# Optimization experiments

Measured on AMD Instinct MI355X. Metric: run time of the kernel, lower is better.

## Reference

```python
import jax, jax.numpy as jnp
import numpy as np

B, T, F, D, K, C, O = 256, 16, 8, 32, 64, 1024, 2

def setup_inputs():
    ks = jax.random.split(jax.random.key(0), 16)
    return {
        "tdata": jax.random.normal(ks[0], (B, T, F, D), jnp.float32),
        "f_mask": jax.random.randint(ks[1], (B, T, F), 0, 2, jnp.int32),
        "centers": jax.random.normal(ks[2], (F, K, D), jnp.float32),
        "pat": jax.random.randint(ks[3], (F, C, F), 0, K + 2, jnp.int32),
        "pat_rep": jax.random.normal(ks[4], (F, C, D), jnp.float32),
        "pos_cnt": jax.random.uniform(ks[5], (F, C), jnp.float32),
        "neg_cnt": jax.random.uniform(ks[6], (F, C), jnp.float32),
        "W_q": jax.random.normal(ks[7], (F, D, D), jnp.float32) * 0.1,
        "b_q": jax.random.normal(ks[8], (F, D), jnp.float32) * 0.1,
        "W_k": jax.random.normal(ks[9], (F, D, D + 1), jnp.float32) * 0.1,
        "b_k": jax.random.normal(ks[10], (F, D), jnp.float32) * 0.1,
        "W_v": jax.random.normal(ks[11], (F, D + 1, D + 1), jnp.float32) * 0.1,
        "b_v": jax.random.normal(ks[12], (F, D + 1), jnp.float32) * 0.1,
        "W_pred": jax.random.normal(ks[13], (O, F * (D + 1)), jnp.float32) * 0.1,
    }

def reference(tdata, f_mask, centers, pat, pat_rep, pos_cnt, neg_cnt,
              W_q, b_q, W_k, b_k, W_v, b_v, W_pred):
    Bv, Tv, Fv, Dv = tdata.shape
    BT = Bv * Tv
    fdata = tdata.reshape(BT, Fv, Dv)                     # [BT, F, D]

    # --- VQ nearest-centroid codes per feature (compute_codes) ---
    def codes_one(x, cen):                                # x [BT, D], cen [K, D]
        d = (jnp.sum(x * x, 1, keepdims=True)
             - 2.0 * (x @ cen.T)
             + jnp.sum(cen * cen, 1)[None, :])
        return jnp.argmin(d, axis=1)
    codes = jax.vmap(codes_one, in_axes=(1, 0), out_axes=1)(fdata, centers)  # [BT, F]
    mflat = f_mask.reshape(BT, Fv)
    # scatter_add equivalent: masked positions get code+2, unmasked get 1
    f_codes = jnp.where(mflat != 0, codes.astype(jnp.int32) + 2, 1)          # [BT, F]

    ratio = pos_cnt / (pos_cnt + neg_cnt + 1e-6)          # [F, C]
    rep = jnp.concatenate([pat_rep, ratio[..., None]], axis=-1)  # [F, C, D+1]
    query = tdata[:, -1]                                  # [B, F, D]

    def per_feature(pat_i, rep_i, q_i, Wq, bq, Wk, bk, Wv, bv):
        # pattern match: wildcard (0) always matches, else code must equal
        wild = pat_i == 0                                 # [C, F]
        eq = jnp.where(wild[None], True, f_codes[:, None, :] == pat_i[None])  # [BT, C, F]
        match = jnp.any(jnp.all(eq, axis=2).reshape(Bv, Tv, -1), axis=1)      # [B, C]
        key_t = match[..., None].astype(rep_i.dtype) * rep_i[None]            # [B, C, D+1]
        iq = q_i @ Wq.T + bq                              # [B, D]
        ik = key_t @ Wk.T + bk                            # [B, C, D]
        iv = key_t @ Wv.T + bv                            # [B, C, D+1]
        e = jnp.einsum('bcd,bd->bc', ik, iq)
        e = e - (1.0 - match.astype(e.dtype)) * 1e7
        a = jax.nn.softmax(e, axis=-1)
        v = jnp.einsum('bc,bcd->bd', a, iv)               # [B, D+1]
        return v, a

    v_all, a_all = jax.vmap(per_feature, in_axes=(0, 0, 1, 0, 0, 0, 0, 0, 0))(
        pat, rep, query, W_q, b_q, W_k, b_k, W_v, b_v)    # [F,B,D+1], [F,B,C]
    srep = jnp.swapaxes(v_all, 0, 1)                      # [B, F, D+1]
    fm = jnp.any(f_mask != 0, axis=1).astype(srep.dtype)  # [B, F]
    srep = srep * fm[..., None]
    cali = srep.reshape(Bv, -1) @ W_pred.T                # [B, O]
    return cali, a_all, srep
```

## Files before the change

### kernel.cpp

```cpp
#include <hip/hip_runtime.h>
#include <math.h>

#define Bv 256
#define Tv 16
#define Fv 8
#define Dv 32
#define Kv 64
#define Cv 1024
#define Ov 2
#define D1 33

typedef unsigned long long u64;
typedef unsigned char u8;

struct SM {
  float xsh[Tv * Fv * Dv];
  u64   cds[Tv];
  int   fmask[Tv * Fv];
  float srep_all[Fv * D1];
  float vsum[Fv][D1];
};

__global__ __launch_bounds__(512) void fused(
    const float* __restrict__ tdata, const int* __restrict__ f_mask,
    const float* __restrict__ centers, const int* __restrict__ pat,
    const float* __restrict__ pat_rep, const float* __restrict__ pos_cnt,
    const float* __restrict__ neg_cnt,
    const float* __restrict__ W_q, const float* __restrict__ b_q,
    const float* __restrict__ W_k, const float* __restrict__ b_k,
    const float* __restrict__ W_v, const float* __restrict__ b_v,
    const float* __restrict__ W_pred,
    float* __restrict__ cali, float* __restrict__ a_out,
    float* __restrict__ srep_out) {
  __shared__ SM sm;
  int b = blockIdx.x, tid = threadIdx.x;
  int w = tid >> 6, lane = tid & 63;

  {
    const float4* src = (const float4*)(tdata + (size_t)b * (Tv * Fv * Dv));
    float4* dst = (float4*)sm.xsh;
    dst[tid] = src[tid];
    dst[tid + 512] = src[tid + 512];
    if (tid < Tv * Fv) sm.fmask[tid] = f_mask[b * (Tv * Fv) + tid];
  }
  __syncthreads();

  {
    const float4* cp = (const float4*)(centers + (size_t)(w * Kv + lane) * Dv);
    float4 c4[8];
    float cc = 0.f;
    #pragma unroll
    for (int i = 0; i < 8; i++) {
      float4 v = cp[i];
      c4[i] = v;
      cc += v.x * v.x + v.y * v.y + v.z * v.z + v.w * v.w;
    }
    #pragma unroll
    for (int t = 0; t < Tv; t += 2) {
      const float4* x0 = (const float4*)&sm.xsh[(t * Fv + w) * Dv];
      const float4* x1 = (const float4*)&sm.xsh[((t + 1) * Fv + w) * Dv];
      float dot0 = 0.f, dot1 = 0.f;
      #pragma unroll
      for (int i = 0; i < 8; i++) {
        float4 a = x0[i], bq = x1[i];
        dot0 += c4[i].x * a.x + c4[i].y * a.y + c4[i].z * a.z + c4[i].w * a.w;
        dot1 += c4[i].x * bq.x + c4[i].y * bq.y + c4[i].z * bq.z + c4[i].w * bq.w;
      }
      float d0 = cc - 2.0f * dot0;
      float d1 = cc - 2.0f * dot1;
      float m0 = d0, m1 = d1;
      #pragma unroll
      for (int off = 1; off <= 32; off <<= 1) {
        m0 = fminf(m0, __shfl_xor(m0, off, 64));
        m1 = fminf(m1, __shfl_xor(m1, off, 64));
      }
      u64 bl0 = __ballot(d0 == m0);
      u64 bl1 = __ballot(d1 == m1);
      int k0 = __ffsll(bl0) - 1;
      int k1 = __ffsll(bl1) - 1;
      if (lane == 0) {
        ((u8*)sm.cds)[t * Fv + w] = sm.fmask[t * Fv + w] ? (u8)(k0 + 2) : (u8)1;
        ((u8*)sm.cds)[(t + 1) * Fv + w] = sm.fmask[(t + 1) * Fv + w] ? (u8)(k1 + 2) : (u8)1;
      }
    }
  }
  __syncthreads();

  int f = w;
  u64 creg[Tv];
  #pragma unroll
  for (int t = 0; t < Tv; t++) creg[t] = sm.cds[t];

  int fmlv = (lane < Tv) ? sm.fmask[lane * Fv + f] : 0;
  bool fm = __any(fmlv != 0);

  unsigned mask16 = 0u;
  #pragma unroll 4
  for (int jj = 0; jj < 16; jj++) {
    int c = (jj << 6) + lane;
    const int4* pr = (const int4*)(pat + ((size_t)f * Cv + c) * Fv);
    int4 pa = pr[0], pb = pr[1];
    int vals[8] = {pa.x, pa.y, pa.z, pa.w, pb.x, pb.y, pb.z, pb.w};
    u64 P = 0, M = 0;
    #pragma unroll
    for (int k = 0; k < 8; k++) {
      P |= ((u64)(vals[k] & 0xFF)) << (8 * k);
      if (vals[k] != 0) M |= 0xFFull << (8 * k);
    }
    u64 pm = P & M;
    bool m = false;
    #pragma unroll
    for (int t = 0; t < Tv; t++) m = m || ((creg[t] & M) == pm);
    if (m) mask16 |= (1u << jj);
  }
  bool anym = __any(mask16 != 0u);

  float* arow = a_out + (size_t)(f * Bv + b) * Cv;

  if (!anym) {
    const float uu = 1.0f / 1024.0f;
    #pragma unroll
    for (int jj = 0; jj < 16; jj++) arow[(jj << 6) + lane] = uu;
    if (lane < D1) {
      float vd = fm ? b_v[f * D1 + lane] : 0.f;
      srep_out[(b * Fv + f) * D1 + lane] = vd;
      sm.srep_all[f * D1 + lane] = vd;
    }
  } else {
    if (lane < D1) sm.vsum[f][lane] = 0.f;
    float iqv = 0.f;
    if (lane < Dv) {
      const float* wq = W_q + (f * Dv + lane) * Dv;
      const float* xq = &sm.xsh[((Tv - 1) * Fv + f) * Dv];
      float s = b_q[f * Dv + lane];
      for (int j = 0; j < Dv; j++) s += wq[j] * xq[j];
      iqv = s;
    }
    float zv = 0.f;
    for (int i = 0; i < Dv; i++) {
      float iqi = __shfl(iqv, i, 64);
      float coef = 0.f;
      if (lane < D1) coef = W_k[(f * Dv + i) * D1 + lane];
      else if (lane == D1) coef = b_k[f * Dv + i];
      zv += coef * iqi;
    }
    float ev[16];
    float lmax = -INFINITY;
    for (int jj = 0; jj < 16; jj++) {
      ev[jj] = 0.f;
      if (mask16 & (1u << jj)) {
        int c = (jj << 6) + lane;
        const float* rp = pat_rep + ((size_t)f * Cv + c) * Dv;
        float p = pos_cnt[f * Cv + c], n = neg_cnt[f * Cv + c];
        float r = p / (p + n + 1e-6f);
        float s = __shfl(zv, D1, 64) + r * __shfl(zv, Dv, 64);
        for (int j = 0; j < Dv; j++) s += rp[j] * __shfl(zv, j, 64);
        ev[jj] = s;
        lmax = fmaxf(lmax, s);
      }
    }
    float bm = lmax;
    #pragma unroll
    for (int off = 1; off <= 32; off <<= 1) bm = fmaxf(bm, __shfl_xor(bm, off, 64));
    float ls = 0.f;
    for (int jj = 0; jj < 16; jj++) {
      if (mask16 & (1u << jj)) { ev[jj] = expf(ev[jj] - bm); ls += ev[jj]; }
    }
    float Zs = ls;
    #pragma unroll
    for (int off = 1; off <= 32; off <<= 1) Zs += __shfl_xor(Zs, off, 64);
    for (int jj = 0; jj < 16; jj++) {
      int c = (jj << 6) + lane;
      bool hit = (mask16 & (1u << jj)) != 0u;
      float a = hit ? ev[jj] / Zs : 0.f;
      arow[c] = a;
      if (hit && a != 0.f) {
        const float* rp = pat_rep + ((size_t)f * Cv + c) * Dv;
        float p = pos_cnt[f * Cv + c], n = neg_cnt[f * Cv + c];
        float r = p / (p + n + 1e-6f);
        for (int j = 0; j < Dv; j++) atomicAdd(&sm.vsum[f][j], a * rp[j]);
        atomicAdd(&sm.vsum[f][Dv], a * r);
      }
    }
    if (lane < D1) {
      float s = b_v[f * D1 + lane];
      const float* wvp = W_v + (f * D1 + lane) * D1;
      for (int j = 0; j < D1; j++) s += wvp[j] * sm.vsum[f][j];
      float vd = fm ? s : 0.f;
      srep_out[(b * Fv + f) * D1 + lane] = vd;
      sm.srep_all[f * D1 + lane] = vd;
    }
  }

  __syncthreads();
  if (tid < 64) {
    int o = tid >> 5, l = tid & 31;
    const float* wp = W_pred + o * (Fv * D1);
    float acc = 0.f;
    for (int i = l; i < Fv * D1; i += 32) acc += sm.srep_all[i] * wp[i];
    #pragma unroll
    for (int off = 16; off >= 1; off >>= 1) acc += __shfl_xor(acc, off, 64);
    if (l == 0) cali[b * Ov + o] = acc;
  }
}

extern "C" void kernel_launch(void* const* d_in, const int* in_sizes, int n_in,
                              void* d_out, int out_size, void* d_ws, size_t ws_size,
                              hipStream_t stream) {
  const float* tdata   = (const float*)d_in[0];
  const int*   f_mask  = (const int*)d_in[1];
  const float* centers = (const float*)d_in[2];
  const int*   pat     = (const int*)d_in[3];
  const float* pat_rep = (const float*)d_in[4];
  const float* pos_cnt = (const float*)d_in[5];
  const float* neg_cnt = (const float*)d_in[6];
  const float* W_q     = (const float*)d_in[7];
  const float* b_q     = (const float*)d_in[8];
  const float* W_k     = (const float*)d_in[9];
  const float* b_k     = (const float*)d_in[10];
  const float* W_v     = (const float*)d_in[11];
  const float* b_v     = (const float*)d_in[12];
  const float* W_pred  = (const float*)d_in[13];

  float* out = (float*)d_out;
  float* cali = out;
  float* a_all = out + (Bv * Ov);
  float* srep = out + (Bv * Ov) + (Fv * (size_t)Bv * Cv);

  fused<<<Bv, 512, 0, stream>>>(
      tdata, f_mask, centers, pat, pat_rep, pos_cnt, neg_cnt,
      W_q, b_q, W_k, b_k, W_v, b_v, W_pred,
      cali, a_all, srep);
}
```

Before: 101.7 us.

## Double block size to split VQ codes and pattern matching across two wave halves

Launches 1024 threads per block so each feature gets two wavefronts, each handling half of the timesteps for VQ code computation and half of the patterns for the match scan. The any-match flag is now combined through shared memory with an extra barrier. The uniform-write fallback is split across both halves. The matched path stays on half 0, which recomputes the full 16-chunk mask. The intent is to shorten the serial work per wave and raise parallelism with only 256 blocks. The cost is duplicated pattern loads in the matched case and an added sync.

```diff
diff --git a/kernel.cpp b/kernel.cpp
--- a/kernel.cpp
+++ b/kernel.cpp
@@ -17,11 +17,12 @@
   float xsh[Tv * Fv * Dv];
   u64   cds[Tv];
   int   fmask[Tv * Fv];
+  int   anyf[Fv][2];
   float srep_all[Fv * D1];
   float vsum[Fv][D1];
 };
 
-__global__ __launch_bounds__(512) void fused(
+__global__ __launch_bounds__(1024) void fused(
     const float* __restrict__ tdata, const int* __restrict__ f_mask,
     const float* __restrict__ centers, const int* __restrict__ pat,
     const float* __restrict__ pat_rep, const float* __restrict__ pos_cnt,
@@ -35,18 +36,17 @@
   __shared__ SM sm;
   int b = blockIdx.x, tid = threadIdx.x;
   int w = tid >> 6, lane = tid & 63;
+  int f = w & 7, half = w >> 3;
 
   {
     const float4* src = (const float4*)(tdata + (size_t)b * (Tv * Fv * Dv));
-    float4* dst = (float4*)sm.xsh;
-    dst[tid] = src[tid];
-    dst[tid + 512] = src[tid + 512];
+    ((float4*)sm.xsh)[tid] = src[tid];
     if (tid < Tv * Fv) sm.fmask[tid] = f_mask[b * (Tv * Fv) + tid];
   }
   __syncthreads();
 
   {
-    const float4* cp = (const float4*)(centers + (size_t)(w * Kv + lane) * Dv);
+    const float4* cp = (const float4*)(centers + (size_t)(f * Kv + lane) * Dv);
     float4 c4[8];
     float cc = 0.f;
     #pragma unroll
@@ -55,10 +55,12 @@
       c4[i] = v;
       cc += v.x * v.x + v.y * v.y + v.z * v.z + v.w * v.w;
     }
-    #pragma unroll
-    for (int t = 0; t < Tv; t += 2) {
-      const float4* x0 = (const float4*)&sm.xsh[(t * Fv + w) * Dv];
-      const float4* x1 = (const float4*)&sm.xsh[((t + 1) * Fv + w) * Dv];
+    int t0 = half * 8;
+    #pragma unroll
+    for (int tt = 0; tt < 8; tt += 2) {
+      int t = t0 + tt;
+      const float4* x0 = (const float4*)&sm.xsh[(t * Fv + f) * Dv];
+      const float4* x1 = (const float4*)&sm.xsh[((t + 1) * Fv + f) * Dv];
       float dot0 = 0.f, dot1 = 0.f;
       #pragma unroll
       for (int i = 0; i < 8; i++) {
@@ -79,14 +81,13 @@
       int k0 = __ffsll(bl0) - 1;
       int k1 = __ffsll(bl1) - 1;
       if (lane == 0) {
-        ((u8*)sm.cds)[t * Fv + w] = sm.fmask[t * Fv + w] ? (u8)(k0 + 2) : (u8)1;
-        ((u8*)sm.cds)[(t + 1) * Fv + w] = sm.fmask[(t + 1) * Fv + w] ? (u8)(k1 + 2) : (u8)1;
-      }
-    }
-  }
-  __syncthreads();
-
-  int f = w;
+        ((u8*)sm.cds)[t * Fv + f] = sm.fmask[t * Fv + f] ? (u8)(k0 + 2) : (u8)1;
+        ((u8*)sm.cds)[(t + 1) * Fv + f] = sm.fmask[(t + 1) * Fv + f] ? (u8)(k1 + 2) : (u8)1;
+      }
+    }
+  }
+  __syncthreads();
+
   u64 creg[Tv];
   #pragma unroll
   for (int t = 0; t < Tv; t++) creg[t] = sm.cds[t];
@@ -94,10 +95,11 @@
   int fmlv = (lane < Tv) ? sm.fmask[lane * Fv + f] : 0;
   bool fm = __any(fmlv != 0);
 
-  unsigned mask16 = 0u;
-  #pragma unroll 4
-  for (int jj = 0; jj < 16; jj++) {
-    int c = (jj << 6) + lane;
+  unsigned mask8 = 0u;
+  #pragma unroll
+  for (int jj = 0; jj < 8; jj++) {
+    int jj2 = half * 8 + jj;
+    int c = (jj2 << 6) + lane;
     const int4* pr = (const int4*)(pat + ((size_t)f * Cv + c) * Fv);
     int4 pa = pr[0], pb = pr[1];
     int vals[8] = {pa.x, pa.y, pa.z, pa.w, pb.x, pb.y, pb.z, pb.w};
@@ -111,22 +113,44 @@
     bool m = false;
     #pragma unroll
     for (int t = 0; t < Tv; t++) m = m || ((creg[t] & M) == pm);
-    if (m) mask16 |= (1u << jj);
-  }
-  bool anym = __any(mask16 != 0u);
+    if (m) mask8 |= (1u << jj);
+  }
+  bool anyw = __any(mask8 != 0u);
+  if (lane == 0) sm.anyf[f][half] = anyw ? 1 : 0;
+  __syncthreads();
+  bool anym = (sm.anyf[f][0] | sm.anyf[f][1]) != 0;
 
   float* arow = a_out + (size_t)(f * Bv + b) * Cv;
 
   if (!anym) {
     const float uu = 1.0f / 1024.0f;
     #pragma unroll
-    for (int jj = 0; jj < 16; jj++) arow[(jj << 6) + lane] = uu;
-    if (lane < D1) {
+    for (int jj = 0; jj < 8; jj++) arow[((half * 8 + jj) << 6) + lane] = uu;
+    if (half == 0 && lane < D1) {
       float vd = fm ? b_v[f * D1 + lane] : 0.f;
       srep_out[(b * Fv + f) * D1 + lane] = vd;
       sm.srep_all[f * D1 + lane] = vd;
     }
-  } else {
+  } else if (half == 0) {
+    unsigned mask16 = 0u;
+    #pragma unroll 4
+    for (int jj = 0; jj < 16; jj++) {
+      int c = (jj << 6) + lane;
+      const int4* pr = (const int4*)(pat + ((size_t)f * Cv + c) * Fv);
+      int4 pa = pr[0], pb = pr[1];
+      int vals[8] = {pa.x, pa.y, pa.z, pa.w, pb.x, pb.y, pb.z, pb.w};
+      u64 P = 0, M = 0;
+      #pragma unroll
+      for (int k = 0; k < 8; k++) {
+        P |= ((u64)(vals[k] & 0xFF)) << (8 * k);
+        if (vals[k] != 0) M |= 0xFFull << (8 * k);
+      }
+      u64 pm = P & M;
+      bool m = false;
+      #pragma unroll
+      for (int t = 0; t < Tv; t++) m = m || ((creg[t] & M) == pm);
+      if (m) mask16 |= (1u << jj);
+    }
     if (lane < D1) sm.vsum[f][lane] = 0.f;
     float iqv = 0.f;
     if (lane < Dv) {
@@ -227,7 +251,7 @@
   float* a_all = out + (Bv * Ov);
   float* srep = out + (Bv * Ov) + (Fv * (size_t)Bv * Cv);
 
-  fused<<<Bv, 512, 0, stream>>>(
+  fused<<<Bv, 1024, 0, stream>>>(
       tdata, f_mask, centers, pat, pat_rep, pos_cnt, neg_cnt,
       W_q, b_q, W_k, b_k, W_v, b_v, W_pred,
       cali, a_all, srep);
```

New measurement: 101.8 us. Within noise of the previous version (+0.2%).
